# Kernel optimization log

Hardware: AMD Instinct MI355X
Metric: run time of the kernel (lower is better)

Reference implementation:

```python
import jax, jax.numpy as jnp
import numpy as np


def setup_inputs() -> dict:
    key = jax.random.key(0)
    x = jax.random.normal(key, (1024, 65536), dtype=jnp.float32)
    return {"x": x, "k": 64}


def reference(x, k):
    # BatchTopK: ReLU, then keep the k*batch largest activations across the
    # ENTIRE flattened batch, zeroing everything else.
    acts = jax.nn.relu(x)
    flat = acts.reshape(-1)                      # [batch * d_sae]
    k_total = k * x.shape[0]
    vals, idx = jax.lax.top_k(flat, k_total)     # global selection
    out = jnp.zeros_like(flat).at[idx].set(vals) # scatter back
    return out.reshape(acts.shape)
```

## Files before the change

kernel.cpp:

```cpp
#include <hip/hip_runtime.h>
#include <stdint.h>


#define HDR_CURSOR 0
#define HDR_FLAG   1
#define HDR_THR    2
#define HDR_ICUT   3
#define HIST_OFF   4096
#define CAND_OFF   16384
#define NBINS      2048u
#define BUCKET_CAP 6144u
#define SCAN_STAGE 1024
#define ROWS       1024u
#define SPEC       3.0f
#define BASE_BITS  0x40400000u

__device__ __forceinline__ uint32_t bin_of(uint32_t key) {
  uint32_t off = key - BASE_BITS;
  uint32_t b = off >> 12;
  return b < NBINS ? b : (NBINS - 1u);
}

__device__ __forceinline__ float max4(float4 a) {
  return fmaxf(fmaxf(a.x, a.y), fmaxf(a.z, a.w));
}

__global__ void k_init(uint32_t* hdr, uint32_t* ghist, uint32_t force_flag) {
  for (uint32_t i = threadIdx.x; i < 64u + NBINS; i += 256u) {
    if (i < 64u) hdr[i] = 0u;
    else ghist[i - 64u] = 0u;
  }
  if (threadIdx.x == 0u) hdr[HDR_FLAG] = force_flag;
}

__device__ __forceinline__ void push4(float4 a, uint32_t gi,
                                      uint32_t* s_cnt, uint2* s_buf) {
  if (a.x >= SPEC) { uint32_t p = atomicAdd(s_cnt, 1u); if (p < SCAN_STAGE) s_buf[p] = make_uint2(__float_as_uint(a.x), gi); }
  if (a.y >= SPEC) { uint32_t p = atomicAdd(s_cnt, 1u); if (p < SCAN_STAGE) s_buf[p] = make_uint2(__float_as_uint(a.y), gi + 1u); }
  if (a.z >= SPEC) { uint32_t p = atomicAdd(s_cnt, 1u); if (p < SCAN_STAGE) s_buf[p] = make_uint2(__float_as_uint(a.z), gi + 2u); }
  if (a.w >= SPEC) { uint32_t p = atomicAdd(s_cnt, 1u); if (p < SCAN_STAGE) s_buf[p] = make_uint2(__float_as_uint(a.w), gi + 3u); }
}

__global__ __launch_bounds__(256) void k_scan(
    const float4* __restrict__ x4, const float* __restrict__ x,
    uint2* __restrict__ cand, uint32_t* __restrict__ hdr,
    uint32_t* __restrict__ ghist,
    uint32_t cap, uint32_t n4, uint32_t n) {
  __shared__ uint32_t s_cnt;
  __shared__ uint32_t s_base;
  __shared__ uint2 s_buf[SCAN_STAGE];
  if (threadIdx.x == 0u) s_cnt = 0u;
  __syncthreads();

  uint32_t nthreads = gridDim.x * blockDim.x;
  uint32_t npair = n4 >> 1;
  for (uint32_t g = blockIdx.x * blockDim.x + threadIdx.x; g < npair; g += nthreads) {
    float4 a = x4[2u * g];
    float4 b = x4[2u * g + 1u];
    float m = fmaxf(max4(a), max4(b));
    if (__ballot(m >= SPEC)) {
      push4(a, 8u * g, &s_cnt, s_buf);
      push4(b, 8u * g + 4u, &s_cnt, s_buf);
    }
  }
  if (blockIdx.x == 0u && (n4 & 1u) && threadIdx.x == 0u) {
    float4 a = x4[n4 - 1u];
    if (max4(a) >= SPEC) push4(a, (n4 - 1u) * 4u, &s_cnt, s_buf);
  }
  uint32_t tail0 = n4 * 4u;
  if (blockIdx.x == 0u && threadIdx.x < (n - tail0)) {
    uint32_t gi = tail0 + threadIdx.x;
    float v = x[gi];
    if (v >= SPEC) { uint32_t p = atomicAdd(&s_cnt, 1u); if (p < SCAN_STAGE) s_buf[p] = make_uint2(__float_as_uint(v), gi); }
  }
  __syncthreads();
  uint32_t cnt = s_cnt;
  if (cnt == 0u) return;
  uint32_t wcnt = cnt < (uint32_t)SCAN_STAGE ? cnt : (uint32_t)SCAN_STAGE;
  if (threadIdx.x == 0u) {
    s_base = atomicAdd(&hdr[HDR_CURSOR], cnt);
    if (cnt > (uint32_t)SCAN_STAGE) atomicOr(&hdr[HDR_FLAG], 1u);
  }
  __syncthreads();
  uint32_t base = s_base;
  for (uint32_t j = threadIdx.x; j < wcnt; j += blockDim.x) {
    uint32_t gidx = base + j;
    if (gidx < cap) {
      uint2 c = s_buf[j];
      cand[gidx] = c;
      atomicAdd(&ghist[bin_of(c.x)], 1u);
    }
  }
  if (threadIdx.x == 0u && base + wcnt > cap) atomicOr(&hdr[HDR_FLAG], 1u);
}

__global__ __launch_bounds__(1024) void k_select(
    const uint2* __restrict__ cand, uint32_t* __restrict__ hdr,
    const uint32_t* __restrict__ ghist,
    const int* __restrict__ kptr, uint32_t cap) {
  __shared__ uint32_t h[NBINS];
  __shared__ uint32_t s_sel, s_rank, s_bcnt;
  __shared__ uint2 bkt[BUCKET_CAP];
  uint32_t tid = threadIdx.x;
  uint32_t K = (uint32_t)kptr[0] * ROWS;
  uint32_t M = hdr[HDR_CURSOR];
  if (hdr[HDR_FLAG] != 0u || M > cap || M < K) {
    if (tid == 0u) hdr[HDR_FLAG] = 1u;
    return;
  }
  if (K == 0u) {
    if (tid == 0u) { hdr[HDR_THR] = 0xFFFFFFFFu; hdr[HDR_ICUT] = 0xFFFFFFFFu; }
    return;
  }
  h[tid] = ghist[tid];
  h[tid + 1024u] = ghist[tid + 1024u];
  if (tid == 0u) s_bcnt = 0u;
  __syncthreads();
  if (tid < 64u) {
    uint32_t seg = NBINS >> 6;
    uint32_t base = tid * seg;
    uint32_t lanesum = 0u;
    for (uint32_t j = 0; j < seg; ++j) lanesum += h[base + j];
    uint32_t s = lanesum;
    for (int d = 1; d < 64; d <<= 1) {
      uint32_t v = (uint32_t)__shfl_down((int)s, d, 64);
      if ((int)tid + d < 64) s += v;
    }
    uint32_t above = s - lanesum;
    if (above < K && above + lanesum >= K) {
      uint32_t r = K - above;
      uint32_t cum = 0u;
      for (int j = (int)seg - 1; j >= 0; --j) {
        uint32_t c = h[base + (uint32_t)j];
        if (cum + c >= r) { s_sel = base + (uint32_t)j; s_rank = r - cum; break; }
        cum += c;
      }
    }
  }
  __syncthreads();
  uint32_t bsel = s_sel;
  uint32_t r = s_rank;
  uint32_t E = h[bsel];
  if (bsel == NBINS - 1u || E > BUCKET_CAP) {
    if (tid == 0u) hdr[HDR_FLAG] = 1u;
    return;
  }
  const uint4* __restrict__ cand4 = (const uint4*)cand;
  uint32_t M2 = M >> 1;
  uint32_t j = tid;
  for (; j + 3072u < M2; j += 4096u) {
    uint4 c0 = cand4[j];
    uint4 c1 = cand4[j + 1024u];
    uint4 c2 = cand4[j + 2048u];
    uint4 c3 = cand4[j + 3072u];
    if (bin_of(c0.x) == bsel) { uint32_t p = atomicAdd(&s_bcnt, 1u); if (p < BUCKET_CAP) bkt[p] = make_uint2(c0.x, c0.y); }
    if (bin_of(c0.z) == bsel) { uint32_t p = atomicAdd(&s_bcnt, 1u); if (p < BUCKET_CAP) bkt[p] = make_uint2(c0.z, c0.w); }
    if (bin_of(c1.x) == bsel) { uint32_t p = atomicAdd(&s_bcnt, 1u); if (p < BUCKET_CAP) bkt[p] = make_uint2(c1.x, c1.y); }
    if (bin_of(c1.z) == bsel) { uint32_t p = atomicAdd(&s_bcnt, 1u); if (p < BUCKET_CAP) bkt[p] = make_uint2(c1.z, c1.w); }
    if (bin_of(c2.x) == bsel) { uint32_t p = atomicAdd(&s_bcnt, 1u); if (p < BUCKET_CAP) bkt[p] = make_uint2(c2.x, c2.y); }
    if (bin_of(c2.z) == bsel) { uint32_t p = atomicAdd(&s_bcnt, 1u); if (p < BUCKET_CAP) bkt[p] = make_uint2(c2.z, c2.w); }
    if (bin_of(c3.x) == bsel) { uint32_t p = atomicAdd(&s_bcnt, 1u); if (p < BUCKET_CAP) bkt[p] = make_uint2(c3.x, c3.y); }
    if (bin_of(c3.z) == bsel) { uint32_t p = atomicAdd(&s_bcnt, 1u); if (p < BUCKET_CAP) bkt[p] = make_uint2(c3.z, c3.w); }
  }
  for (; j < M2; j += 1024u) {
    uint4 c = cand4[j];
    if (bin_of(c.x) == bsel) { uint32_t p = atomicAdd(&s_bcnt, 1u); if (p < BUCKET_CAP) bkt[p] = make_uint2(c.x, c.y); }
    if (bin_of(c.z) == bsel) { uint32_t p = atomicAdd(&s_bcnt, 1u); if (p < BUCKET_CAP) bkt[p] = make_uint2(c.z, c.w); }
  }
  if (tid == 0u && (M & 1u)) {
    uint2 c = cand[M - 1u];
    if (bin_of(c.x) == bsel) { uint32_t p = atomicAdd(&s_bcnt, 1u); if (p < BUCKET_CAP) bkt[p] = c; }
  }
  __syncthreads();
  for (uint32_t e = tid; e < E; e += 1024u) {
    uint2 me = bkt[e];
    uint32_t rank = 0u;
    for (uint32_t jj = 0; jj < E; ++jj) {
      uint2 o = bkt[jj];
      rank += (o.x > me.x || (o.x == me.x && o.y < me.y)) ? 1u : 0u;
    }
    if (rank == r - 1u) { hdr[HDR_THR] = me.x; hdr[HDR_ICUT] = me.y; }
  }
}

__global__ __launch_bounds__(256) void k_scatter(
    const uint2* __restrict__ cand, const uint32_t* __restrict__ hdr,
    float* __restrict__ out, uint32_t cap) {
  if (hdr[HDR_FLAG] != 0u) return;
  uint32_t M = hdr[HDR_CURSOR]; if (M > cap) M = cap;
  uint32_t thr = hdr[HDR_THR], icut = hdr[HDR_ICUT];
  uint32_t stride = gridDim.x * blockDim.x;
  for (uint32_t i = blockIdx.x * blockDim.x + threadIdx.x; i < M; i += stride) {
    uint2 c = cand[i];
    if (c.x > thr || (c.x == thr && c.y <= icut)) out[c.y] = __uint_as_float(c.x);
  }
}

__global__ __launch_bounds__(1024) void k_fallback(
    const float* __restrict__ x, float* __restrict__ out,
    const int* __restrict__ kptr, const uint32_t* __restrict__ hdr, uint32_t n) {
  if (hdr[HDR_FLAG] == 0u) return;
  __shared__ uint32_t hist[2048];
  __shared__ uint32_t s_sel, s_rank, s_found, s_eqcnt, s_icut;
  __shared__ uint32_t eq_idx[4096];
  uint32_t tid = threadIdx.x;
  uint32_t K = (uint32_t)kptr[0] * ROWS;
  uint32_t prefix = 0u;
  uint32_t R = K;
  bool zero_thr = (K == 0u);
  for (int lvl = 0; lvl < 3 && !zero_thr; ++lvl) {
    uint32_t shift = (lvl == 0) ? 21u : (lvl == 1 ? 10u : 0u);
    uint32_t nb = (lvl == 2) ? 1024u : 2048u;
    for (uint32_t b = tid; b < nb; b += 1024u) hist[b] = 0u;
    __syncthreads();
    for (uint32_t i = tid; i < n; i += 1024u) {
      float v = x[i];
      uint32_t key = (v > 0.f) ? __float_as_uint(v) : 0u;
      bool valid = (key != 0u);
      if (lvl == 1) valid = valid && ((key >> 21) == prefix);
      if (lvl == 2) valid = valid && ((key >> 10) == prefix);
      if (valid) atomicAdd(&hist[(key >> shift) & (nb - 1u)], 1u);
    }
    __syncthreads();
    if (tid == 0u) {
      uint32_t cum = 0u, sel = 0u, rr = R, found = 0u;
      for (int b = (int)nb - 1; b >= 0; --b) {
        uint32_t c = hist[b];
        if (cum + c >= R) { sel = (uint32_t)b; rr = R - cum; found = 1u; break; }
        cum += c;
      }
      s_sel = sel; s_rank = rr; s_found = found;
    }
    __syncthreads();
    if (s_found == 0u) {
      zero_thr = true;
    } else {
      uint32_t sel = s_sel;
      R = s_rank;
      if (lvl == 0) prefix = sel;
      else if (lvl == 1) prefix = (prefix << 11) | sel;
      else prefix = (prefix << 10) | sel;
    }
    __syncthreads();
  }
  uint32_t thr_key = zero_thr ? 0u : prefix;
  uint32_t icut = 0xFFFFFFFFu;
  if (!zero_thr) {
    uint32_t E = hist[thr_key & 1023u];
    uint32_t T = R;
    if (T < E) {
      if (tid == 0u) { s_eqcnt = 0u; s_icut = 0xFFFFFFFFu; }
      __syncthreads();
      for (uint32_t i = tid; i < n; i += 1024u) {
        float v = x[i];
        if (v > 0.f && __float_as_uint(v) == thr_key) {
          uint32_t p = atomicAdd(&s_eqcnt, 1u);
          if (p < 4096u) eq_idx[p] = i;
        }
      }
      __syncthreads();
      uint32_t ec = s_eqcnt < 4096u ? s_eqcnt : 4096u;
      for (uint32_t e = tid; e < ec; e += 1024u) {
        uint32_t me = eq_idx[e];
        uint32_t rank = 0u;
        for (uint32_t j = 0; j < ec; ++j) rank += (eq_idx[j] < me) ? 1u : 0u;
        if (rank == T - 1u) s_icut = me;
      }
      __syncthreads();
      icut = s_icut;
    }
  }
  for (uint32_t i = tid; i < n; i += 1024u) {
    float v = x[i];
    uint32_t key = (v > 0.f) ? __float_as_uint(v) : 0u;
    bool keep = (key > thr_key) || (key != 0u && key == thr_key && i <= icut);
    out[i] = keep ? v : 0.f;
  }
}

extern "C" void kernel_launch(void* const* d_in, const int* in_sizes, int n_in,
                              void* d_out, int out_size, void* d_ws, size_t ws_size,
                              hipStream_t stream) {
  const float* x = (const float*)d_in[0];
  const int* kptr = (const int*)d_in[1];
  float* out = (float*)d_out;
  uint32_t n = (uint32_t)in_sizes[0];
  uint32_t n4 = n >> 2;

  uint32_t* hdr = (uint32_t*)d_ws;
  uint32_t* ghist = (uint32_t*)((char*)d_ws + HIST_OFF);
  uint2* cand = (uint2*)((char*)d_ws + CAND_OFF);
  uint32_t cap = (ws_size > (size_t)CAND_OFF) ? (uint32_t)((ws_size - CAND_OFF) / 8) : 0u;
  uint32_t force = (cap < 131072u) ? 1u : 0u;

  k_init<<<1, 256, 0, stream>>>(hdr, ghist, force);
  k_scan<<<2048, 256, 0, stream>>>((const float4*)x, x, cand, hdr, ghist, cap, n4, n);
  hipMemsetAsync(out, 0, (size_t)n * 4u, stream);
  k_select<<<1, 1024, 0, stream>>>(cand, hdr, ghist, kptr, cap);
  k_fallback<<<1, 1024, 0, stream>>>(x, out, kptr, hdr, n);
  k_scatter<<<512, 256, 0, stream>>>(cand, hdr, out, cap);
}
```

Measured before the change: 502.0 us.

## Fuse select and fallback kernels, use wave-chunked scan loads, memset init

The scan loop now has each wavefront process contiguous 256-float4 chunks as four coalesced loads, with a ballot per load instead of a grid-strided pair. The select and fallback kernels are merged into one k_finish kernel that shares a single shared-memory buffer, which removes one launch. On the normal path the header and histogram are zeroed with hipMemsetAsync instead of the init kernel. The change targets per-launch overhead and scan memory efficiency. The trade-offs are larger shared-memory use in the fused kernel and a different memset size assumption for the workspace header.

```diff
diff --git a/kernel.cpp b/kernel.cpp
--- a/kernel.cpp
+++ b/kernel.cpp
@@ -49,41 +49,49 @@
   __shared__ uint32_t s_cnt;
   __shared__ uint32_t s_base;
   __shared__ uint2 s_buf[SCAN_STAGE];
-  if (threadIdx.x == 0u) s_cnt = 0u;
-  __syncthreads();
-
-  uint32_t nthreads = gridDim.x * blockDim.x;
-  uint32_t npair = n4 >> 1;
-  for (uint32_t g = blockIdx.x * blockDim.x + threadIdx.x; g < npair; g += nthreads) {
-    float4 a = x4[2u * g];
-    float4 b = x4[2u * g + 1u];
-    float m = fmaxf(max4(a), max4(b));
-    if (__ballot(m >= SPEC)) {
-      push4(a, 8u * g, &s_cnt, s_buf);
-      push4(b, 8u * g + 4u, &s_cnt, s_buf);
-    }
-  }
-  if (blockIdx.x == 0u && (n4 & 1u) && threadIdx.x == 0u) {
-    float4 a = x4[n4 - 1u];
-    if (max4(a) >= SPEC) push4(a, (n4 - 1u) * 4u, &s_cnt, s_buf);
-  }
-  uint32_t tail0 = n4 * 4u;
-  if (blockIdx.x == 0u && threadIdx.x < (n - tail0)) {
-    uint32_t gi = tail0 + threadIdx.x;
-    float v = x[gi];
-    if (v >= SPEC) { uint32_t p = atomicAdd(&s_cnt, 1u); if (p < SCAN_STAGE) s_buf[p] = make_uint2(__float_as_uint(v), gi); }
+  uint32_t tid = threadIdx.x;
+  if (tid == 0u) s_cnt = 0u;
+  __syncthreads();
+
+  uint32_t lane = tid & 63u;
+  uint32_t gwid = (blockIdx.x * blockDim.x + tid) >> 6;
+  uint32_t nw   = (gridDim.x * blockDim.x) >> 6;
+  uint32_t nchunk = n4 >> 8;
+  for (uint32_t c = gwid; c < nchunk; c += nw) {
+    uint32_t base = c << 8;
+    float4 a0 = x4[base + lane];
+    float4 a1 = x4[base + 64u + lane];
+    float4 a2 = x4[base + 128u + lane];
+    float4 a3 = x4[base + 192u + lane];
+    if (__ballot(max4(a0) >= SPEC)) push4(a0, (base + lane) * 4u, &s_cnt, s_buf);
+    if (__ballot(max4(a1) >= SPEC)) push4(a1, (base + 64u + lane) * 4u, &s_cnt, s_buf);
+    if (__ballot(max4(a2) >= SPEC)) push4(a2, (base + 128u + lane) * 4u, &s_cnt, s_buf);
+    if (__ballot(max4(a3) >= SPEC)) push4(a3, (base + 192u + lane) * 4u, &s_cnt, s_buf);
+  }
+  uint32_t rem0 = nchunk << 8;
+  if (blockIdx.x == 0u) {
+    for (uint32_t i = rem0 + tid; i < n4; i += blockDim.x) {
+      float4 a = x4[i];
+      if (__ballot(max4(a) >= SPEC)) push4(a, i * 4u, &s_cnt, s_buf);
+    }
+    uint32_t tail0 = n4 * 4u;
+    if (tid < (n - tail0)) {
+      uint32_t gi = tail0 + tid;
+      float v = x[gi];
+      if (v >= SPEC) { uint32_t p = atomicAdd(&s_cnt, 1u); if (p < SCAN_STAGE) s_buf[p] = make_uint2(__float_as_uint(v), gi); }
+    }
   }
   __syncthreads();
   uint32_t cnt = s_cnt;
   if (cnt == 0u) return;
   uint32_t wcnt = cnt < (uint32_t)SCAN_STAGE ? cnt : (uint32_t)SCAN_STAGE;
-  if (threadIdx.x == 0u) {
+  if (tid == 0u) {
     s_base = atomicAdd(&hdr[HDR_CURSOR], cnt);
     if (cnt > (uint32_t)SCAN_STAGE) atomicOr(&hdr[HDR_FLAG], 1u);
   }
   __syncthreads();
   uint32_t base = s_base;
-  for (uint32_t j = threadIdx.x; j < wcnt; j += blockDim.x) {
+  for (uint32_t j = tid; j < wcnt; j += blockDim.x) {
     uint32_t gidx = base + j;
     if (gidx < cap) {
       uint2 c = s_buf[j];
@@ -91,95 +99,176 @@
       atomicAdd(&ghist[bin_of(c.x)], 1u);
     }
   }
-  if (threadIdx.x == 0u && base + wcnt > cap) atomicOr(&hdr[HDR_FLAG], 1u);
-}
-
-__global__ __launch_bounds__(1024) void k_select(
+  if (tid == 0u && base + wcnt > cap) atomicOr(&hdr[HDR_FLAG], 1u);
+}
+
+__global__ __launch_bounds__(1024) void k_finish(
     const uint2* __restrict__ cand, uint32_t* __restrict__ hdr,
-    const uint32_t* __restrict__ ghist,
-    const int* __restrict__ kptr, uint32_t cap) {
-  __shared__ uint32_t h[NBINS];
-  __shared__ uint32_t s_sel, s_rank, s_bcnt;
-  __shared__ uint2 bkt[BUCKET_CAP];
+    const uint32_t* __restrict__ ghist, const int* __restrict__ kptr,
+    const float* __restrict__ x, float* __restrict__ out,
+    uint32_t cap, uint32_t n) {
+  __shared__ __align__(16) uint8_t smem[57344];
+  uint32_t* h      = (uint32_t*)smem;
+  uint2*    bkt    = (uint2*)(smem + 8192);
+  uint32_t* eq_idx = (uint32_t*)(smem + 8192);
+  __shared__ uint32_t s_sel, s_rank, s_bcnt, s_need, s_found, s_eqcnt, s_icut;
   uint32_t tid = threadIdx.x;
   uint32_t K = (uint32_t)kptr[0] * ROWS;
   uint32_t M = hdr[HDR_CURSOR];
-  if (hdr[HDR_FLAG] != 0u || M > cap || M < K) {
-    if (tid == 0u) hdr[HDR_FLAG] = 1u;
-    return;
-  }
-  if (K == 0u) {
+  if (tid == 0u) s_need = 0u;
+  __syncthreads();
+
+  bool skip_sel = (hdr[HDR_FLAG] != 0u || M > cap || M < K);
+  if (skip_sel) {
+    if (tid == 0u) s_need = 1u;
+  } else if (K == 0u) {
     if (tid == 0u) { hdr[HDR_THR] = 0xFFFFFFFFu; hdr[HDR_ICUT] = 0xFFFFFFFFu; }
     return;
-  }
-  h[tid] = ghist[tid];
-  h[tid + 1024u] = ghist[tid + 1024u];
-  if (tid == 0u) s_bcnt = 0u;
-  __syncthreads();
-  if (tid < 64u) {
-    uint32_t seg = NBINS >> 6;
-    uint32_t base = tid * seg;
-    uint32_t lanesum = 0u;
-    for (uint32_t j = 0; j < seg; ++j) lanesum += h[base + j];
-    uint32_t s = lanesum;
-    for (int d = 1; d < 64; d <<= 1) {
-      uint32_t v = (uint32_t)__shfl_down((int)s, d, 64);
-      if ((int)tid + d < 64) s += v;
-    }
-    uint32_t above = s - lanesum;
-    if (above < K && above + lanesum >= K) {
-      uint32_t r = K - above;
-      uint32_t cum = 0u;
-      for (int j = (int)seg - 1; j >= 0; --j) {
-        uint32_t c = h[base + (uint32_t)j];
-        if (cum + c >= r) { s_sel = base + (uint32_t)j; s_rank = r - cum; break; }
+  } else {
+    h[tid] = ghist[tid];
+    h[tid + 1024u] = ghist[tid + 1024u];
+    if (tid == 0u) s_bcnt = 0u;
+    __syncthreads();
+    if (tid < 64u) {
+      uint32_t seg = NBINS >> 6;
+      uint32_t base = tid * seg;
+      uint32_t lanesum = 0u;
+      for (uint32_t j = 0; j < seg; ++j) lanesum += h[base + j];
+      uint32_t s = lanesum;
+      for (int d = 1; d < 64; d <<= 1) {
+        uint32_t v = (uint32_t)__shfl_down((int)s, d, 64);
+        if ((int)tid + d < 64) s += v;
+      }
+      uint32_t above = s - lanesum;
+      if (above < K && above + lanesum >= K) {
+        uint32_t r = K - above;
+        uint32_t cum = 0u;
+        for (int j = (int)seg - 1; j >= 0; --j) {
+          uint32_t c = h[base + (uint32_t)j];
+          if (cum + c >= r) { s_sel = base + (uint32_t)j; s_rank = r - cum; break; }
+          cum += c;
+        }
+      }
+    }
+    __syncthreads();
+    uint32_t bsel = s_sel;
+    uint32_t r = s_rank;
+    uint32_t E = h[bsel];
+    if (bsel == NBINS - 1u || E > BUCKET_CAP) {
+      if (tid == 0u) s_need = 1u;
+    } else {
+      const uint4* __restrict__ cand4 = (const uint4*)cand;
+      uint32_t M2 = M >> 1;
+      uint32_t j = tid;
+      for (; j + 3072u < M2; j += 4096u) {
+        uint4 c0 = cand4[j];
+        uint4 c1 = cand4[j + 1024u];
+        uint4 c2 = cand4[j + 2048u];
+        uint4 c3 = cand4[j + 3072u];
+        if (bin_of(c0.x) == bsel) { uint32_t p = atomicAdd(&s_bcnt, 1u); if (p < BUCKET_CAP) bkt[p] = make_uint2(c0.x, c0.y); }
+        if (bin_of(c0.z) == bsel) { uint32_t p = atomicAdd(&s_bcnt, 1u); if (p < BUCKET_CAP) bkt[p] = make_uint2(c0.z, c0.w); }
+        if (bin_of(c1.x) == bsel) { uint32_t p = atomicAdd(&s_bcnt, 1u); if (p < BUCKET_CAP) bkt[p] = make_uint2(c1.x, c1.y); }
+        if (bin_of(c1.z) == bsel) { uint32_t p = atomicAdd(&s_bcnt, 1u); if (p < BUCKET_CAP) bkt[p] = make_uint2(c1.z, c1.w); }
+        if (bin_of(c2.x) == bsel) { uint32_t p = atomicAdd(&s_bcnt, 1u); if (p < BUCKET_CAP) bkt[p] = make_uint2(c2.x, c2.y); }
+        if (bin_of(c2.z) == bsel) { uint32_t p = atomicAdd(&s_bcnt, 1u); if (p < BUCKET_CAP) bkt[p] = make_uint2(c2.z, c2.w); }
+        if (bin_of(c3.x) == bsel) { uint32_t p = atomicAdd(&s_bcnt, 1u); if (p < BUCKET_CAP) bkt[p] = make_uint2(c3.x, c3.y); }
+        if (bin_of(c3.z) == bsel) { uint32_t p = atomicAdd(&s_bcnt, 1u); if (p < BUCKET_CAP) bkt[p] = make_uint2(c3.z, c3.w); }
+      }
+      for (; j < M2; j += 1024u) {
+        uint4 c = cand4[j];
+        if (bin_of(c.x) == bsel) { uint32_t p = atomicAdd(&s_bcnt, 1u); if (p < BUCKET_CAP) bkt[p] = make_uint2(c.x, c.y); }
+        if (bin_of(c.z) == bsel) { uint32_t p = atomicAdd(&s_bcnt, 1u); if (p < BUCKET_CAP) bkt[p] = make_uint2(c.z, c.w); }
+      }
+      if (tid == 0u && (M & 1u)) {
+        uint2 c = cand[M - 1u];
+        if (bin_of(c.x) == bsel) { uint32_t p = atomicAdd(&s_bcnt, 1u); if (p < BUCKET_CAP) bkt[p] = c; }
+      }
+      __syncthreads();
+      for (uint32_t e = tid; e < E; e += 1024u) {
+        uint2 me = bkt[e];
+        uint32_t rank = 0u;
+        for (uint32_t jj = 0; jj < E; ++jj) {
+          uint2 o = bkt[jj];
+          rank += (o.x > me.x || (o.x == me.x && o.y < me.y)) ? 1u : 0u;
+        }
+        if (rank == r - 1u) { hdr[HDR_THR] = me.x; hdr[HDR_ICUT] = me.y; }
+      }
+    }
+  }
+  __syncthreads();
+  if (s_need == 0u) return;
+  if (tid == 0u) hdr[HDR_FLAG] = 1u;
+
+  uint32_t prefix = 0u;
+  uint32_t R = K;
+  bool zero_thr = (K == 0u);
+  for (int lvl = 0; lvl < 3 && !zero_thr; ++lvl) {
+    uint32_t shift = (lvl == 0) ? 21u : (lvl == 1 ? 10u : 0u);
+    uint32_t nb = (lvl == 2) ? 1024u : 2048u;
+    for (uint32_t b = tid; b < nb; b += 1024u) h[b] = 0u;
+    __syncthreads();
+    for (uint32_t i = tid; i < n; i += 1024u) {
+      float v = x[i];
+      uint32_t key = (v > 0.f) ? __float_as_uint(v) : 0u;
+      bool valid = (key != 0u);
+      if (lvl == 1) valid = valid && ((key >> 21) == prefix);
+      if (lvl == 2) valid = valid && ((key >> 10) == prefix);
+      if (valid) atomicAdd(&h[(key >> shift) & (nb - 1u)], 1u);
+    }
+    __syncthreads();
+    if (tid == 0u) {
+      uint32_t cum = 0u, sel = 0u, rr = R, found = 0u;
+      for (int b = (int)nb - 1; b >= 0; --b) {
+        uint32_t c = h[b];
+        if (cum + c >= R) { sel = (uint32_t)b; rr = R - cum; found = 1u; break; }
         cum += c;
       }
-    }
-  }
-  __syncthreads();
-  uint32_t bsel = s_sel;
-  uint32_t r = s_rank;
-  uint32_t E = h[bsel];
-  if (bsel == NBINS - 1u || E > BUCKET_CAP) {
-    if (tid == 0u) hdr[HDR_FLAG] = 1u;
-    return;
-  }
-  const uint4* __restrict__ cand4 = (const uint4*)cand;
-  uint32_t M2 = M >> 1;
-  uint32_t j = tid;
-  for (; j + 3072u < M2; j += 4096u) {
-    uint4 c0 = cand4[j];
-    uint4 c1 = cand4[j + 1024u];
-    uint4 c2 = cand4[j + 2048u];
-    uint4 c3 = cand4[j + 3072u];
-    if (bin_of(c0.x) == bsel) { uint32_t p = atomicAdd(&s_bcnt, 1u); if (p < BUCKET_CAP) bkt[p] = make_uint2(c0.x, c0.y); }
-    if (bin_of(c0.z) == bsel) { uint32_t p = atomicAdd(&s_bcnt, 1u); if (p < BUCKET_CAP) bkt[p] = make_uint2(c0.z, c0.w); }
-    if (bin_of(c1.x) == bsel) { uint32_t p = atomicAdd(&s_bcnt, 1u); if (p < BUCKET_CAP) bkt[p] = make_uint2(c1.x, c1.y); }
-    if (bin_of(c1.z) == bsel) { uint32_t p = atomicAdd(&s_bcnt, 1u); if (p < BUCKET_CAP) bkt[p] = make_uint2(c1.z, c1.w); }
-    if (bin_of(c2.x) == bsel) { uint32_t p = atomicAdd(&s_bcnt, 1u); if (p < BUCKET_CAP) bkt[p] = make_uint2(c2.x, c2.y); }
-    if (bin_of(c2.z) == bsel) { uint32_t p = atomicAdd(&s_bcnt, 1u); if (p < BUCKET_CAP) bkt[p] = make_uint2(c2.z, c2.w); }
-    if (bin_of(c3.x) == bsel) { uint32_t p = atomicAdd(&s_bcnt, 1u); if (p < BUCKET_CAP) bkt[p] = make_uint2(c3.x, c3.y); }
-    if (bin_of(c3.z) == bsel) { uint32_t p = atomicAdd(&s_bcnt, 1u); if (p < BUCKET_CAP) bkt[p] = make_uint2(c3.z, c3.w); }
-  }
-  for (; j < M2; j += 1024u) {
-    uint4 c = cand4[j];
-    if (bin_of(c.x) == bsel) { uint32_t p = atomicAdd(&s_bcnt, 1u); if (p < BUCKET_CAP) bkt[p] = make_uint2(c.x, c.y); }
-    if (bin_of(c.z) == bsel) { uint32_t p = atomicAdd(&s_bcnt, 1u); if (p < BUCKET_CAP) bkt[p] = make_uint2(c.z, c.w); }
-  }
-  if (tid == 0u && (M & 1u)) {
-    uint2 c = cand[M - 1u];
-    if (bin_of(c.x) == bsel) { uint32_t p = atomicAdd(&s_bcnt, 1u); if (p < BUCKET_CAP) bkt[p] = c; }
-  }
-  __syncthreads();
-  for (uint32_t e = tid; e < E; e += 1024u) {
-    uint2 me = bkt[e];
-    uint32_t rank = 0u;
-    for (uint32_t jj = 0; jj < E; ++jj) {
-      uint2 o = bkt[jj];
-      rank += (o.x > me.x || (o.x == me.x && o.y < me.y)) ? 1u : 0u;
-    }
-    if (rank == r - 1u) { hdr[HDR_THR] = me.x; hdr[HDR_ICUT] = me.y; }
+      s_sel = sel; s_rank = rr; s_found = found;
+    }
+    __syncthreads();
+    if (s_found == 0u) {
+      zero_thr = true;
+    } else {
+      uint32_t sel = s_sel;
+      R = s_rank;
+      if (lvl == 0) prefix = sel;
+      else if (lvl == 1) prefix = (prefix << 11) | sel;
+      else prefix = (prefix << 10) | sel;
+    }
+    __syncthreads();
+  }
+  uint32_t thr_key = zero_thr ? 0u : prefix;
+  uint32_t icut = 0xFFFFFFFFu;
+  if (!zero_thr) {
+    uint32_t E2 = h[thr_key & 1023u];
+    uint32_t T = R;
+    if (T < E2) {
+      if (tid == 0u) { s_eqcnt = 0u; s_icut = 0xFFFFFFFFu; }
+      __syncthreads();
+      for (uint32_t i = tid; i < n; i += 1024u) {
+        float v = x[i];
+        if (v > 0.f && __float_as_uint(v) == thr_key) {
+          uint32_t p = atomicAdd(&s_eqcnt, 1u);
+          if (p < 4096u) eq_idx[p] = i;
+        }
+      }
+      __syncthreads();
+      uint32_t ec = s_eqcnt < 4096u ? s_eqcnt : 4096u;
+      for (uint32_t e = tid; e < ec; e += 1024u) {
+        uint32_t me = eq_idx[e];
+        uint32_t rank = 0u;
+        for (uint32_t j = 0; j < ec; ++j) rank += (eq_idx[j] < me) ? 1u : 0u;
+        if (rank == T - 1u) s_icut = me;
+      }
+      __syncthreads();
+      icut = s_icut;
+    }
+  }
+  for (uint32_t i = tid; i < n; i += 1024u) {
+    float v = x[i];
+    uint32_t key = (v > 0.f) ? __float_as_uint(v) : 0u;
+    bool keep = (key > thr_key) || (key != 0u && key == thr_key && i <= icut);
+    out[i] = keep ? v : 0.f;
   }
 }
 
@@ -196,88 +285,6 @@
   }
 }
 
-__global__ __launch_bounds__(1024) void k_fallback(
-    const float* __restrict__ x, float* __restrict__ out,
-    const int* __restrict__ kptr, const uint32_t* __restrict__ hdr, uint32_t n) {
-  if (hdr[HDR_FLAG] == 0u) return;
-  __shared__ uint32_t hist[2048];
-  __shared__ uint32_t s_sel, s_rank, s_found, s_eqcnt, s_icut;
-  __shared__ uint32_t eq_idx[4096];
-  uint32_t tid = threadIdx.x;
-  uint32_t K = (uint32_t)kptr[0] * ROWS;
-  uint32_t prefix = 0u;
-  uint32_t R = K;
-  bool zero_thr = (K == 0u);
-  for (int lvl = 0; lvl < 3 && !zero_thr; ++lvl) {
-    uint32_t shift = (lvl == 0) ? 21u : (lvl == 1 ? 10u : 0u);
-    uint32_t nb = (lvl == 2) ? 1024u : 2048u;
-    for (uint32_t b = tid; b < nb; b += 1024u) hist[b] = 0u;
-    __syncthreads();
-    for (uint32_t i = tid; i < n; i += 1024u) {
-      float v = x[i];
-      uint32_t key = (v > 0.f) ? __float_as_uint(v) : 0u;
-      bool valid = (key != 0u);
-      if (lvl == 1) valid = valid && ((key >> 21) == prefix);
-      if (lvl == 2) valid = valid && ((key >> 10) == prefix);
-      if (valid) atomicAdd(&hist[(key >> shift) & (nb - 1u)], 1u);
-    }
-    __syncthreads();
-    if (tid == 0u) {
-      uint32_t cum = 0u, sel = 0u, rr = R, found = 0u;
-      for (int b = (int)nb - 1; b >= 0; --b) {
-        uint32_t c = hist[b];
-        if (cum + c >= R) { sel = (uint32_t)b; rr = R - cum; found = 1u; break; }
-        cum += c;
-      }
-      s_sel = sel; s_rank = rr; s_found = found;
-    }
-    __syncthreads();
-    if (s_found == 0u) {
-      zero_thr = true;
-    } else {
-      uint32_t sel = s_sel;
-      R = s_rank;
-      if (lvl == 0) prefix = sel;
-      else if (lvl == 1) prefix = (prefix << 11) | sel;
-      else prefix = (prefix << 10) | sel;
-    }
-    __syncthreads();
-  }
-  uint32_t thr_key = zero_thr ? 0u : prefix;
-  uint32_t icut = 0xFFFFFFFFu;
-  if (!zero_thr) {
-    uint32_t E = hist[thr_key & 1023u];
-    uint32_t T = R;
-    if (T < E) {
-      if (tid == 0u) { s_eqcnt = 0u; s_icut = 0xFFFFFFFFu; }
-      __syncthreads();
-      for (uint32_t i = tid; i < n; i += 1024u) {
-        float v = x[i];
-        if (v > 0.f && __float_as_uint(v) == thr_key) {
-          uint32_t p = atomicAdd(&s_eqcnt, 1u);
-          if (p < 4096u) eq_idx[p] = i;
-        }
-      }
-      __syncthreads();
-      uint32_t ec = s_eqcnt < 4096u ? s_eqcnt : 4096u;
-      for (uint32_t e = tid; e < ec; e += 1024u) {
-        uint32_t me = eq_idx[e];
-        uint32_t rank = 0u;
-        for (uint32_t j = 0; j < ec; ++j) rank += (eq_idx[j] < me) ? 1u : 0u;
-        if (rank == T - 1u) s_icut = me;
-      }
-      __syncthreads();
-      icut = s_icut;
-    }
-  }
-  for (uint32_t i = tid; i < n; i += 1024u) {
-    float v = x[i];
-    uint32_t key = (v > 0.f) ? __float_as_uint(v) : 0u;
-    bool keep = (key > thr_key) || (key != 0u && key == thr_key && i <= icut);
-    out[i] = keep ? v : 0.f;
-  }
-}
-
 extern "C" void kernel_launch(void* const* d_in, const int* in_sizes, int n_in,
                               void* d_out, int out_size, void* d_ws, size_t ws_size,
                               hipStream_t stream) {
@@ -291,12 +298,14 @@
   uint32_t* ghist = (uint32_t*)((char*)d_ws + HIST_OFF);
   uint2* cand = (uint2*)((char*)d_ws + CAND_OFF);
   uint32_t cap = (ws_size > (size_t)CAND_OFF) ? (uint32_t)((ws_size - CAND_OFF) / 8) : 0u;
-  uint32_t force = (cap < 131072u) ? 1u : 0u;
-
-  k_init<<<1, 256, 0, stream>>>(hdr, ghist, force);
+
+  if (cap < 131072u) {
+    k_init<<<1, 256, 0, stream>>>(hdr, ghist, 1u);
+  } else {
+    hipMemsetAsync(d_ws, 0, 12288, stream);
+  }
   k_scan<<<2048, 256, 0, stream>>>((const float4*)x, x, cand, hdr, ghist, cap, n4, n);
   hipMemsetAsync(out, 0, (size_t)n * 4u, stream);
-  k_select<<<1, 1024, 0, stream>>>(cand, hdr, ghist, kptr, cap);
-  k_fallback<<<1, 1024, 0, stream>>>(x, out, kptr, hdr, n);
+  k_finish<<<1, 1024, 0, stream>>>(cand, hdr, ghist, kptr, x, out, cap, n);
   k_scatter<<<512, 256, 0, stream>>>(cand, hdr, out, cap);
 }
```

New measurement: 484.8 us. 3.4% less time.
